# Kernel optimization log

Hardware: AMD Instinct MI355X
Metric: run time of the kernel (lower is better)

## Reference

```python
import jax, jax.numpy as jnp
import numpy as np
jax.config.update("jax_enable_x64", True)

BASE = [2654435761, 2246822519, 3266489917, 2028178513, 1220703125, 1610612741, 805306457, 402653189,
        3674653429, 2860486313, 1073676287, 2971215073, 1500450271, 3267000013, 2654435789, 4049292737]
EXT32 = BASE + [2246822531, 3266489927, 2028178519, 1220703133, 1610612759, 805306463, 402653201, 3674653441,
                2860486319, 1073676311, 2971215091, 1500450277, 3267000023, 2654435801, 4049292751, 2246822537]
HASH_PRIMES = [
    BASE[:1], BASE[:2], BASE[:4], BASE[:8], BASE[:16],
    [p ^ 3735928559 for p in EXT32],
    [p ^ 3405691582 for p in (BASE[:8] * 8)],
    [p ^ 2343432205 for p in (BASE[:8] * 16)],
]
SCALE_WINDOWS = [1, 2, 4, 8, 16, 32, 64, 128]
BUCKETS = 65536
NUM_SCALES = 8
E = 16
BOUNDARY = 4
SIGN_BITS = 8
COND_PRIMES = BASE[:SIGN_BITS]


def _hash_scale(tokens, scale_idx):
    # tokens: [B, T] int64. Rolling polynomial hash over a window of past tokens.
    T = tokens.shape[1]
    primes = HASH_PRIMES[scale_idx][:SCALE_WINDOWS[scale_idx]]
    h = jnp.zeros_like(tokens)
    for i, p in enumerate(primes):
        off = i + 1
        if off >= T:
            continue
        shifted = jnp.pad(tokens[:, :-off], ((0, 0), (off, 0)))  # shift right by off
        h = h ^ (shifted * p)
    return h % BUCKETS


def setup_inputs() -> dict:
    key = jax.random.key(0)
    k1, k2, k3 = jax.random.split(key, 3)
    B, T = 32, 4096
    tokens = jax.random.randint(k1, (B, T), 0, 1024, dtype=jnp.int64)
    tables = (0.02 * jax.random.normal(k2, (NUM_SCALES, BUCKETS, E))).astype(jnp.float32)
    Wc = (0.02 * jax.random.normal(k3, (SIGN_BITS, BOUNDARY * E))).astype(jnp.float32)
    return {"tokens": tokens, "tables": tables, "Wc": Wc}


def reference(tokens, tables, Wc):
    keys = [_hash_scale(tokens, s) for s in range(NUM_SCALES)]  # each [B, T] int64 in [0, BUCKETS)
    # short-range scale embeddings
    short = [tables[s][keys[s]] for s in range(BOUNDARY)]  # each [B, T, E]
    short_cat = jnp.concatenate(short, axis=-1)            # [B, T, BOUNDARY*E]
    cond_logits = short_cat @ Wc.T                         # [B, T, SIGN_BITS]
    sign_bits = (cond_logits > 0).astype(jnp.int64)
    cond_key = jnp.zeros(tokens.shape, dtype=jnp.int64)
    for i in range(SIGN_BITS):
        cond_key = cond_key ^ (sign_bits[:, :, i] * COND_PRIMES[i])
    long = [tables[s][(keys[s] ^ cond_key) % BUCKETS] for s in range(BOUNDARY, NUM_SCALES)]
    return jnp.stack(short + long, axis=2)  # [B, T, NUM_SCALES, E]
```

## Files before the change

### kernel.cpp

```cpp
#include <hip/hip_runtime.h>

typedef unsigned int u32;

__device__ constexpr u32 BASEP[16] = {
    2654435761u, 2246822519u, 3266489917u, 2028178513u,
    1220703125u, 1610612741u,  805306457u,  402653189u,
    3674653429u, 2860486313u, 1073676287u, 2971215073u,
    1500450271u, 3267000013u, 2654435789u, 4049292737u};
__device__ constexpr u32 EXTP[16] = {
    2246822531u, 3266489927u, 2028178519u, 1220703133u,
    1610612759u,  805306463u,  402653201u, 3674653441u,
    2860486319u, 1073676311u, 2971215091u, 1500450277u,
    3267000023u, 2654435801u, 4049292751u, 2246822537u};

#define TDIM 4096
#define PPB  16
#define HALO 128

__global__ __launch_bounds__(256) void rhp_fused(
        const int* __restrict__ tokens, const float* __restrict__ tables,
        const float* __restrict__ Wc, float* __restrict__ out)
{
    __shared__ u32   toks[HALO + PPB];
    __shared__ float wc_s[512];
    __shared__ u32   bp16[16], ep16[16];

    const int tid = threadIdx.x;
    const int g0  = blockIdx.x * PPB;
    const int t0  = g0 & (TDIM - 1);

    if (tid < 16) { bp16[tid] = BASEP[tid] & 0xFFFFu;
                    ep16[tid] = EXTP[tid]  & 0xFFFFu; }
    if (tid < 128) ((float4*)wc_s)[tid] = ((const float4*)Wc)[tid];
    if (tid < HALO + PPB) {
        const int t = t0 - HALO + tid;
        toks[tid] = (t >= 0) ? (u32)tokens[g0 - HALO + tid] : 0u;
    }
    __syncthreads();

    const int r   = tid & 15;
    const int p   = tid >> 4;
    const int pos = g0 + p;
    const int s   = (tid >> 2) & 3;
    const int q   = tid & 3;

    const int base = HALO + p - 1 - r;
    const u32 v0 = toks[base      ], v1 = toks[base -  16];
    const u32 v2 = toks[base -  32], v3 = toks[base -  48];
    const u32 v4 = toks[base -  64], v5 = toks[base -  80];
    const u32 v6 = toks[base -  96], v7 = toks[base - 112];

    const u32 pb  = bp16[r];
    const u32 pb7 = bp16[r & 7];
    const u32 pe  = ep16[r];
    const u32 p7  = pb7 ^ 0xF00Du;
    const u32 p6  = pb7 ^ 0xBABEu;
    const u32 p5a = pb  ^ 0xBEEFu;
    const u32 p5b = pe  ^ 0xBEEFu;

    u32 k7p = __umul24(v0, p7) ^ __umul24(v1, p7) ^ __umul24(v2, p7) ^
              __umul24(v3, p7) ^ __umul24(v4, p7) ^ __umul24(v5, p7) ^
              __umul24(v6, p7) ^ __umul24(v7, p7);
    u32 k6p = __umul24(v0, p6) ^ __umul24(v1, p6) ^
              __umul24(v2, p6) ^ __umul24(v3, p6);
    u32 k5p = __umul24(v0, p5a) ^ __umul24(v1, p5b);
    u32 k4p = __umul24(v0, pb);
    const u32 k3p = (r < 8) ? k4p : 0u;
    const u32 k2p = (r < 4) ? k4p : 0u;
    const u32 k1p = (r < 2) ? k4p : 0u;
    const u32 k0p = (r == 0) ? k4p : 0u;

    u32 P0 = (k0p & 0xFFFFu) | ((k4p & 0xFFFFu) << 16);
    u32 P1 = (k1p & 0xFFFFu) | ((k5p & 0xFFFFu) << 16);
    u32 P2 = (k2p & 0xFFFFu) | ((k6p & 0xFFFFu) << 16);
    u32 P3 = (k3p & 0xFFFFu) | ((k7p & 0xFFFFu) << 16);
#pragma unroll
    for (int d = 1; d <= 8; d <<= 1) {
        P0 ^= __shfl_xor(P0, d);
        P1 ^= __shfl_xor(P1, d);
        P2 ^= __shfl_xor(P2, d);
        P3 ^= __shfl_xor(P3, d);
    }
    const u32 Ps = (s == 0) ? P0 : (s == 1) ? P1 : (s == 2) ? P2 : P3;
    const u32 ks = Ps & 0xFFFFu;

    const float4 sv = *(const float4*)(tables + (u32)s * 1048576u
                                       + ks * 16u + (u32)q * 4u);
    *(float4*)(out + (size_t)pos * 128u + (u32)s * 16u + (u32)q * 4u) = sv;

    float lg[8];
#pragma unroll
    for (int j = 0; j < 8; ++j) {
        const float4 w = ((const float4*)wc_s)[j * 16 + s * 4 + q];
        lg[j] = fmaf(sv.x, w.x, fmaf(sv.y, w.y, fmaf(sv.z, w.z, sv.w * w.w)));
    }
#pragma unroll
    for (int d = 1; d <= 8; d <<= 1) {
#pragma unroll
        for (int j = 0; j < 8; ++j) lg[j] += __shfl_xor(lg[j], d);
    }

    u32 ck = 0u;
#pragma unroll
    for (int j = 0; j < 8; ++j)
        if (lg[j] > 0.0f) ck ^= (BASEP[j] & 0xFFFFu);

    const u32 kl = ((Ps >> 16) ^ ck) & 0xFFFFu;
    const float4 lv = *(const float4*)(tables + (u32)(s + 4) * 1048576u
                                       + kl * 16u + (u32)q * 4u);
    *(float4*)(out + (size_t)pos * 128u + 64u + (u32)s * 16u + (u32)q * 4u) = lv;
}

extern "C" void kernel_launch(void* const* d_in, const int* in_sizes, int n_in,
                              void* d_out, int out_size, void* d_ws, size_t ws_size,
                              hipStream_t stream) {
    const int*   tokens = (const int*)d_in[0];
    const float* tables = (const float*)d_in[1];
    const float* Wc     = (const float*)d_in[2];
    float*       out    = (float*)d_out;

    const int n_pos = in_sizes[0];
    hipLaunchKernelGGL(rhp_fused, dim3(n_pos / PPB), dim3(256), 0, stream,
                       tokens, tables, Wc, out);
}
```

Baseline: 110.4 us.

## Process four position groups per block with DPP butterfly reductions

Each block now handles 64 positions instead of 16. A 4-iteration loop reuses the shared token window by shifting the sliding register window, and the Wc weights are hoisted into registers once per thread. The 16-lane xor and sum reductions now use DPP row operations instead of ds_swizzle/bpermute shuffles, which cuts LDS traffic and latency. The trade-off is fewer blocks, so less parallelism to hide the latency of the serial gathers inside each thread.

```diff
diff --git a/kernel.cpp b/kernel.cpp
--- a/kernel.cpp
+++ b/kernel.cpp
@@ -14,14 +14,43 @@
     3267000023u, 2654435801u, 4049292751u, 2246822537u};
 
 #define TDIM 4096
-#define PPB  16
+#define PPB  64
 #define HALO 128
+#define NTOK (HALO + PPB)
+
+__device__ __forceinline__ int dpp_x1(int x) {
+    return __builtin_amdgcn_update_dpp(0, x, 0xB1, 0xF, 0xF, true);
+}
+__device__ __forceinline__ int dpp_x2(int x) {
+    return __builtin_amdgcn_update_dpp(0, x, 0x4E, 0xF, 0xF, true);
+}
+__device__ __forceinline__ int dpp_x4(int x) {
+    int y = __builtin_amdgcn_update_dpp(0, x, 0x104, 0xF, 0x5, false);
+    return  __builtin_amdgcn_update_dpp(y, x, 0x114, 0xF, 0xA, false);
+}
+__device__ __forceinline__ int dpp_x8(int x) {
+    return __builtin_amdgcn_update_dpp(0, x, 0x128, 0xF, 0xF, true);
+}
+__device__ __forceinline__ u32 bxor16(u32 x) {
+    x ^= (u32)dpp_x1((int)x);
+    x ^= (u32)dpp_x2((int)x);
+    x ^= (u32)dpp_x4((int)x);
+    x ^= (u32)dpp_x8((int)x);
+    return x;
+}
+__device__ __forceinline__ float fsum16(float x) {
+    x += __int_as_float(dpp_x1(__float_as_int(x)));
+    x += __int_as_float(dpp_x2(__float_as_int(x)));
+    x += __int_as_float(dpp_x4(__float_as_int(x)));
+    x += __int_as_float(dpp_x8(__float_as_int(x)));
+    return x;
+}
 
 __global__ __launch_bounds__(256) void rhp_fused(
         const int* __restrict__ tokens, const float* __restrict__ tables,
         const float* __restrict__ Wc, float* __restrict__ out)
 {
-    __shared__ u32   toks[HALO + PPB];
+    __shared__ u32   toks[NTOK];
     __shared__ float wc_s[512];
     __shared__ u32   bp16[16], ep16[16];
 
@@ -32,23 +61,20 @@
     if (tid < 16) { bp16[tid] = BASEP[tid] & 0xFFFFu;
                     ep16[tid] = EXTP[tid]  & 0xFFFFu; }
     if (tid < 128) ((float4*)wc_s)[tid] = ((const float4*)Wc)[tid];
-    if (tid < HALO + PPB) {
+    if (tid < NTOK) {
         const int t = t0 - HALO + tid;
         toks[tid] = (t >= 0) ? (u32)tokens[g0 - HALO + tid] : 0u;
     }
     __syncthreads();
 
-    const int r   = tid & 15;
-    const int p   = tid >> 4;
-    const int pos = g0 + p;
-    const int s   = (tid >> 2) & 3;
-    const int q   = tid & 3;
+    const int r    = tid & 15;
+    const int slot = tid >> 4;
+    const int s    = (tid >> 2) & 3;
+    const int q    = tid & 3;
 
-    const int base = HALO + p - 1 - r;
-    const u32 v0 = toks[base      ], v1 = toks[base -  16];
-    const u32 v2 = toks[base -  32], v3 = toks[base -  48];
-    const u32 v4 = toks[base -  64], v5 = toks[base -  80];
-    const u32 v6 = toks[base -  96], v7 = toks[base - 112];
+    float4 w[8];
+#pragma unroll
+    for (int j = 0; j < 8; ++j) w[j] = ((const float4*)wc_s)[j * 16 + s * 4 + q];
 
     const u32 pb  = bp16[r];
     const u32 pb7 = bp16[r & 7];
@@ -58,57 +84,66 @@
     const u32 p5a = pb  ^ 0xBEEFu;
     const u32 p5b = pe  ^ 0xBEEFu;
 
-    u32 k7p = __umul24(v0, p7) ^ __umul24(v1, p7) ^ __umul24(v2, p7) ^
-              __umul24(v3, p7) ^ __umul24(v4, p7) ^ __umul24(v5, p7) ^
-              __umul24(v6, p7) ^ __umul24(v7, p7);
-    u32 k6p = __umul24(v0, p6) ^ __umul24(v1, p6) ^
-              __umul24(v2, p6) ^ __umul24(v3, p6);
-    u32 k5p = __umul24(v0, p5a) ^ __umul24(v1, p5b);
-    u32 k4p = __umul24(v0, pb);
-    const u32 k3p = (r < 8) ? k4p : 0u;
-    const u32 k2p = (r < 4) ? k4p : 0u;
-    const u32 k1p = (r < 2) ? k4p : 0u;
-    const u32 k0p = (r == 0) ? k4p : 0u;
+    const int base = HALO - 1 + slot - r;
+    u32 v0 = toks[base      ], v1 = toks[base -  16];
+    u32 v2 = toks[base -  32], v3 = toks[base -  48];
+    u32 v4 = toks[base -  64], v5 = toks[base -  80];
+    u32 v6 = toks[base -  96], v7 = toks[base - 112];
 
-    u32 P0 = (k0p & 0xFFFFu) | ((k4p & 0xFFFFu) << 16);
-    u32 P1 = (k1p & 0xFFFFu) | ((k5p & 0xFFFFu) << 16);
-    u32 P2 = (k2p & 0xFFFFu) | ((k6p & 0xFFFFu) << 16);
-    u32 P3 = (k3p & 0xFFFFu) | ((k7p & 0xFFFFu) << 16);
+    const float* tshort = tables + (u32)s * 1048576u + (u32)q * 4u;
+    const float* tlong  = tshort + 4u * 1048576u;
+    float* o = out + (size_t)(g0 + slot) * 128u + (u32)s * 16u + (u32)q * 4u;
+
 #pragma unroll
-    for (int d = 1; d <= 8; d <<= 1) {
-        P0 ^= __shfl_xor(P0, d);
-        P1 ^= __shfl_xor(P1, d);
-        P2 ^= __shfl_xor(P2, d);
-        P3 ^= __shfl_xor(P3, d);
+    for (int it = 0; it < 4; ++it) {
+        u32 k7 = __umul24(v0, p7) ^ __umul24(v1, p7) ^ __umul24(v2, p7) ^
+                 __umul24(v3, p7) ^ __umul24(v4, p7) ^ __umul24(v5, p7) ^
+                 __umul24(v6, p7) ^ __umul24(v7, p7);
+        u32 k6 = __umul24(v0, p6) ^ __umul24(v1, p6) ^
+                 __umul24(v2, p6) ^ __umul24(v3, p6);
+        u32 k5 = __umul24(v0, p5a) ^ __umul24(v1, p5b);
+        u32 k4 = __umul24(v0, pb);
+        const u32 k3 = (r < 8) ? k4 : 0u;
+        const u32 k2 = (r < 4) ? k4 : 0u;
+        const u32 k1 = (r < 2) ? k4 : 0u;
+        const u32 k0 = (r == 0) ? k4 : 0u;
+
+        u32 P0 = (k0 & 0xFFFFu) | ((k4 & 0xFFFFu) << 16);
+        u32 P1 = (k1 & 0xFFFFu) | ((k5 & 0xFFFFu) << 16);
+        u32 P2 = (k2 & 0xFFFFu) | ((k6 & 0xFFFFu) << 16);
+        u32 P3 = (k3 & 0xFFFFu) | ((k7 & 0xFFFFu) << 16);
+        P0 = bxor16(P0); P1 = bxor16(P1); P2 = bxor16(P2); P3 = bxor16(P3);
+
+        const u32 Ps = (s == 0) ? P0 : (s == 1) ? P1 : (s == 2) ? P2 : P3;
+        const u32 ks = Ps & 0xFFFFu;
+
+        const float4 sv = *(const float4*)(tshort + ks * 16u);
+        *(float4*)o = sv;
+
+        float lg[8];
+#pragma unroll
+        for (int j = 0; j < 8; ++j)
+            lg[j] = fmaf(sv.x, w[j].x, fmaf(sv.y, w[j].y,
+                     fmaf(sv.z, w[j].z, sv.w * w[j].w)));
+#pragma unroll
+        for (int j = 0; j < 8; ++j) lg[j] = fsum16(lg[j]);
+
+        u32 ck = 0u;
+#pragma unroll
+        for (int j = 0; j < 8; ++j)
+            if (lg[j] > 0.0f) ck ^= (BASEP[j] & 0xFFFFu);
+
+        const u32 kl = ((Ps >> 16) ^ ck) & 0xFFFFu;
+        const float4 lv = *(const float4*)(tlong + kl * 16u);
+        *(float4*)(o + 64u) = lv;
+
+        if (it < 3) {
+            v7 = v6; v6 = v5; v5 = v4; v4 = v3;
+            v3 = v2; v2 = v1; v1 = v0;
+            v0 = toks[base + 16 * (it + 1)];
+            o += 16 * 128;
+        }
     }
-    const u32 Ps = (s == 0) ? P0 : (s == 1) ? P1 : (s == 2) ? P2 : P3;
-    const u32 ks = Ps & 0xFFFFu;
-
-    const float4 sv = *(const float4*)(tables + (u32)s * 1048576u
-                                       + ks * 16u + (u32)q * 4u);
-    *(float4*)(out + (size_t)pos * 128u + (u32)s * 16u + (u32)q * 4u) = sv;
-
-    float lg[8];
-#pragma unroll
-    for (int j = 0; j < 8; ++j) {
-        const float4 w = ((const float4*)wc_s)[j * 16 + s * 4 + q];
-        lg[j] = fmaf(sv.x, w.x, fmaf(sv.y, w.y, fmaf(sv.z, w.z, sv.w * w.w)));
-    }
-#pragma unroll
-    for (int d = 1; d <= 8; d <<= 1) {
-#pragma unroll
-        for (int j = 0; j < 8; ++j) lg[j] += __shfl_xor(lg[j], d);
-    }
-
-    u32 ck = 0u;
-#pragma unroll
-    for (int j = 0; j < 8; ++j)
-        if (lg[j] > 0.0f) ck ^= (BASEP[j] & 0xFFFFu);
-
-    const u32 kl = ((Ps >> 16) ^ ck) & 0xFFFFu;
-    const float4 lv = *(const float4*)(tables + (u32)(s + 4) * 1048576u
-                                       + kl * 16u + (u32)q * 4u);
-    *(float4*)(out + (size_t)pos * 128u + 64u + (u32)s * 16u + (u32)q * 4u) = lv;
 }
 
 extern "C" void kernel_launch(void* const* d_in, const int* in_sizes, int n_in,
```

After: 109.3 us. No clear change (-1.0%).

## Use DPP cross-lane reductions, nontemporal output stores, and occupancy hint

Applied to the files above, without the earlier changes.

Replaces the __shfl_xor butterfly reductions over 16-lane groups with DPP-based XOR and sum reductions (quad_perm, row_shr/shl with bank masks, row_mirror), avoiding LDS-routed ds_bpermute shuffles. Output stores become nontemporal so the write-once output does not displace table lines in cache. Launch bounds gain a minimum-blocks hint of 8. The DPP lane patterns must exactly reproduce the xor-1/2/4/8 butterfly, or results could silently change.

```diff
diff --git a/kernel.cpp b/kernel.cpp
--- a/kernel.cpp
+++ b/kernel.cpp
@@ -1,6 +1,7 @@
 #include <hip/hip_runtime.h>
 
 typedef unsigned int u32;
+typedef float f4 __attribute__((ext_vector_type(4)));
 
 __device__ constexpr u32 BASEP[16] = {
     2654435761u, 2246822519u, 3266489917u, 2028178513u,
@@ -16,12 +17,41 @@
 #define TDIM 4096
 #define PPB  16
 #define HALO 128
+#define NTOK (HALO + PPB)
 
-__global__ __launch_bounds__(256) void rhp_fused(
+__device__ __forceinline__ int dpp_x1(int x) {
+    return __builtin_amdgcn_update_dpp(0, x, 0xB1, 0xF, 0xF, true);
+}
+__device__ __forceinline__ int dpp_x2(int x) {
+    return __builtin_amdgcn_update_dpp(0, x, 0x4E, 0xF, 0xF, true);
+}
+__device__ __forceinline__ int dpp_x4(int x) {
+    int y = __builtin_amdgcn_update_dpp(0, x, 0x104, 0xF, 0x5, false);
+    return  __builtin_amdgcn_update_dpp(y, x, 0x114, 0xF, 0xA, false);
+}
+__device__ __forceinline__ int dpp_x8(int x) {
+    return __builtin_amdgcn_update_dpp(0, x, 0x128, 0xF, 0xF, true);
+}
+__device__ __forceinline__ u32 bxor16(u32 x) {
+    x ^= (u32)dpp_x1((int)x);
+    x ^= (u32)dpp_x2((int)x);
+    x ^= (u32)dpp_x4((int)x);
+    x ^= (u32)dpp_x8((int)x);
+    return x;
+}
+__device__ __forceinline__ float fsum16(float x) {
+    x += __int_as_float(dpp_x1(__float_as_int(x)));
+    x += __int_as_float(dpp_x2(__float_as_int(x)));
+    x += __int_as_float(dpp_x4(__float_as_int(x)));
+    x += __int_as_float(dpp_x8(__float_as_int(x)));
+    return x;
+}
+
+__global__ __launch_bounds__(256, 8) void rhp_fused(
         const int* __restrict__ tokens, const float* __restrict__ tables,
         const float* __restrict__ Wc, float* __restrict__ out)
 {
-    __shared__ u32   toks[HALO + PPB];
+    __shared__ u32   toks[NTOK];
     __shared__ float wc_s[512];
     __shared__ u32   bp16[16], ep16[16];
 
@@ -32,7 +62,7 @@
     if (tid < 16) { bp16[tid] = BASEP[tid] & 0xFFFFu;
                     ep16[tid] = EXTP[tid]  & 0xFFFFu; }
     if (tid < 128) ((float4*)wc_s)[tid] = ((const float4*)Wc)[tid];
-    if (tid < HALO + PPB) {
+    if (tid < NTOK) {
         const int t = t0 - HALO + tid;
         toks[tid] = (t >= 0) ? (u32)tokens[g0 - HALO + tid] : 0u;
     }
@@ -74,19 +104,13 @@
     u32 P1 = (k1p & 0xFFFFu) | ((k5p & 0xFFFFu) << 16);
     u32 P2 = (k2p & 0xFFFFu) | ((k6p & 0xFFFFu) << 16);
     u32 P3 = (k3p & 0xFFFFu) | ((k7p & 0xFFFFu) << 16);
-#pragma unroll
-    for (int d = 1; d <= 8; d <<= 1) {
-        P0 ^= __shfl_xor(P0, d);
-        P1 ^= __shfl_xor(P1, d);
-        P2 ^= __shfl_xor(P2, d);
-        P3 ^= __shfl_xor(P3, d);
-    }
+    P0 = bxor16(P0); P1 = bxor16(P1); P2 = bxor16(P2); P3 = bxor16(P3);
     const u32 Ps = (s == 0) ? P0 : (s == 1) ? P1 : (s == 2) ? P2 : P3;
     const u32 ks = Ps & 0xFFFFu;
 
-    const float4 sv = *(const float4*)(tables + (u32)s * 1048576u
-                                       + ks * 16u + (u32)q * 4u);
-    *(float4*)(out + (size_t)pos * 128u + (u32)s * 16u + (u32)q * 4u) = sv;
+    const float* tshort = tables + (u32)s * 1048576u + (u32)q * 4u;
+    float* o = out + (size_t)pos * 128u + (u32)s * 16u + (u32)q * 4u;
+    const float4 sv = *(const float4*)(tshort + ks * 16u);
 
     float lg[8];
 #pragma unroll
@@ -94,11 +118,10 @@
         const float4 w = ((const float4*)wc_s)[j * 16 + s * 4 + q];
         lg[j] = fmaf(sv.x, w.x, fmaf(sv.y, w.y, fmaf(sv.z, w.z, sv.w * w.w)));
     }
+    __builtin_nontemporal_store((f4){sv.x, sv.y, sv.z, sv.w}, (f4*)o);
+
 #pragma unroll
-    for (int d = 1; d <= 8; d <<= 1) {
-#pragma unroll
-        for (int j = 0; j < 8; ++j) lg[j] += __shfl_xor(lg[j], d);
-    }
+    for (int j = 0; j < 8; ++j) lg[j] = fsum16(lg[j]);
 
     u32 ck = 0u;
 #pragma unroll
@@ -106,9 +129,8 @@
         if (lg[j] > 0.0f) ck ^= (BASEP[j] & 0xFFFFu);
 
     const u32 kl = ((Ps >> 16) ^ ck) & 0xFFFFu;
-    const float4 lv = *(const float4*)(tables + (u32)(s + 4) * 1048576u
-                                       + kl * 16u + (u32)q * 4u);
-    *(float4*)(out + (size_t)pos * 128u + 64u + (u32)s * 16u + (u32)q * 4u) = lv;
+    const float4 lv = *(const float4*)(tshort + 4u * 1048576u + kl * 16u);
+    __builtin_nontemporal_store((f4){lv.x, lv.y, lv.z, lv.w}, (f4*)(o + 64u));
 }
 
 extern "C" void kernel_launch(void* const* d_in, const int* in_sizes, int n_in,
```

Measured after the change: 110.0 us. About the same (-0.3%).
